# Kernel tuning notes

Hardware: AMD Instinct MI355X
Metric: run time of the kernel (lower is better)

The kernel has to match this reference:

```python
import jax, jax.numpy as jnp
import numpy as np

HEADS = 8
KS = 7
PAD = 3


def grouped_conv1x1(x, w):
    # x: (B, Cin, H, W), w: (heads, Cout/h, Cin/h) -> (B, Cout, H, W)
    B, Cin, H, W = x.shape
    g, co, ci = w.shape
    xg = x.reshape(B, g, ci, H, W)
    out = jnp.einsum('bgchw,goc->bgohw', xg, w)
    return out.reshape(B, g * co, H, W)


def unfold2d(p, k):
    # p: (B, C, Hp, Wp) -> (B, C, H, W, k, k) sliding windows, stride 1
    B, C, Hp, Wp = p.shape
    H, W = Hp - k + 1, Wp - k + 1
    rows = [jnp.stack([p[:, :, i:i + H, j:j + W] for j in range(k)], axis=-1)
            for i in range(k)]
    return jnp.stack(rows, axis=-2)  # (B,C,H,W,k,k)


def setup_inputs() -> dict:
    key = jax.random.key(0)
    ks = jax.random.split(key, 7)
    B, Cin, H, W = 8, 64, 64, 64
    Cout = 64
    g = HEADS
    return {
        'x': jax.random.normal(ks[0], (B, Cin, H, W), jnp.float32),
        'r': jax.random.normal(ks[1], (1,), jnp.float32),
        'w_q': jax.random.normal(ks[2], (g, Cout // g, Cin // g), jnp.float32) * 0.2,
        'w_k': jax.random.normal(ks[3], (g, Cout // g, Cin // g), jnp.float32) * 0.2,
        'w_v': jax.random.normal(ks[4], (g, Cout // g, Cin // g), jnp.float32) * 0.2,
        'rel_h': jax.random.normal(ks[5], (Cout // 2, KS), jnp.float32),
        'rel_w': jax.random.normal(ks[6], (Cout // 2, KS), jnp.float32),
    }


def reference(x, r, w_q, w_k, w_v, rel_h, rel_w):
    B, Cin, H, W = x.shape
    g = HEADS
    Cout = w_q.shape[0] * w_q.shape[1]
    dh = Cout // g

    padded = jnp.pad(x, ((0, 0), (0, 0), (PAD, PAD), (PAD, PAD)))
    q = grouped_conv1x1(x, w_q)            # (B, Cout, H, W)
    k = grouped_conv1x1(padded, w_k)       # (B, Cout, H+2p, W+2p)
    v = grouped_conv1x1(padded, w_v)

    k = unfold2d(k, KS)                    # (B, Cout, H, W, KS, KS)
    v = unfold2d(v, KS)

    # learnable relative positional encoding: split channels in half,
    # add rel_h along window-height, rel_w along window-width
    half = Cout // 2
    k_h = k[:, :half] + rel_h[None, :, None, None, :, None]
    k_w = k[:, half:] + rel_w[None, :, None, None, None, :]
    k = jnp.concatenate([k_h, k_w], axis=1)

    K2 = KS * KS
    k = k.reshape(B, g, dh, H, W, K2)
    v = v.reshape(B, g, dh, H, W, K2)
    q = q.reshape(B, g, dh, H, W, 1)

    scale = np.sqrt(g / Cout).astype(np.float32)
    logits = (q * k).sum(axis=2, keepdims=True) * scale   # (B,g,1,H,W,K2)
    attn = jax.nn.softmax(logits, axis=-1)
    out = (attn * v).sum(axis=-1)                          # (B,g,dh,H,W)
    return out.reshape(B, Cout, H, W)
```

## Files before the change

kernel.cpp:

```cpp
#include <hip/hip_runtime.h>
#include <math.h>

#define NG  8
#define DH  8
#define NCP 4
#define KS  7
#define PAD 3
#define TH  16
#define TW  32
#define OW  2
#define TPH 22
#define RSTW 40
#define PLW  (TPH * RSTW)
#define CH  64
#define HH  64
#define WW  64

typedef __fp16 h2v __attribute__((ext_vector_type(2)));
typedef __fp16 h4v __attribute__((ext_vector_type(4)));

#if __has_builtin(__builtin_amdgcn_exp2f)
#define EXP2(x) __builtin_amdgcn_exp2f(x)
#else
#define EXP2(x) exp2f(x)
#endif

__device__ __forceinline__ int imin(int a, int b) { return a < b ? a : b; }
__device__ __forceinline__ int imax(int a, int b) { return a > b ? a : b; }

__global__ __launch_bounds__(256, 2)
void saconv_kernel(const float* __restrict__ x,
                   const float* __restrict__ wq,
                   const float* __restrict__ wk,
                   const float* __restrict__ wv,
                   const float* __restrict__ relh,
                   const float* __restrict__ relw,
                   float* __restrict__ out) {
  __shared__ h2v xs2[NCP * PLW];
  __shared__ h2v swq2[DH * NCP];
  __shared__ h2v swv2[DH * NCP];
  __shared__ h2v swk2[DH * NCP];
  __shared__ h2v srel2[KS * NCP];

  const int tx  = threadIdx.x;
  const int ty  = threadIdx.y;
  const int tid = ty * 16 + tx;
  const int bz  = blockIdx.z;
  const int b   = bz >> 3;
  const int g   = bz & 7;
  const int h0  = blockIdx.y * TH;
  const int w0  = blockIdx.x * TW;

  const float sl2e = 0.35355339059327373f * 1.4426950408889634f;

  if (tid < 32) {
    int c = tid >> 2, cp = tid & 3;
    swq2[tid] = __builtin_amdgcn_cvt_pkrtz(wq[g * 64 + c * 8 + 2 * cp],
                                           wq[g * 64 + c * 8 + 2 * cp + 1]);
  } else if (tid < 64) {
    int t2 = tid - 32;
    int c = t2 >> 2, cp = t2 & 3;
    swv2[t2] = __builtin_amdgcn_cvt_pkrtz(wv[g * 64 + c * 8 + 2 * cp],
                                          wv[g * 64 + c * 8 + 2 * cp + 1]);
  } else if (tid < 96) {
    int t2 = tid - 64;
    int ci = t2 >> 2, cP = t2 & 3;
    swk2[t2] = __builtin_amdgcn_cvt_pkrtz(wk[g * 64 + (2 * cP) * 8 + ci] * sl2e,
                                          wk[g * 64 + (2 * cP + 1) * 8 + ci] * sl2e);
  } else if (tid < 96 + KS * NCP) {
    int t2 = tid - 96;
    int t = t2 >> 2, cP = t2 & 3;
    float a0, a1;
    if (g < 4) {
      a0 = relh[(g * 8 + 2 * cP) * KS + t];
      a1 = relh[(g * 8 + 2 * cP + 1) * KS + t];
    } else {
      a0 = relw[((g - 4) * 8 + 2 * cP) * KS + t];
      a1 = relw[((g - 4) * 8 + 2 * cP + 1) * KS + t];
    }
    srel2[t2] = __builtin_amdgcn_cvt_pkrtz(a0 * sl2e, a1 * sl2e);
  }

  const float* xb = x + (size_t)(b * CH + g * DH) * (HH * WW);
  const int NCHK = NCP * TPH * 19;
  #pragma unroll
  for (int kk = 0; kk < 7; kk++) {
    int f = tid + kk * 256;
    if (f < NCHK) {
      int cp  = f / (TPH * 19);
      int r   = f - cp * (TPH * 19);
      int row = r / 19;
      int cc  = r - row * 19;
      int yy  = h0 + row - PAD;
      int cy  = imin(imax(yy, 0), HH - 1);
      bool yok = (yy >= 0) & (yy < HH);
      const float* p0 = xb + ((size_t)(2 * cp) * HH + cy) * WW;
      float v0[2], v1[2];
      #pragma unroll
      for (int e = 0; e < 2; e++) {
        int xx = w0 + 2 * cc + e - PAD;
        int cx = imin(imax(xx, 0), WW - 1);
        bool inb = yok & (xx >= 0) & (xx < WW);
        float a0 = p0[cx];
        float a1 = p0[HH * WW + cx];
        v0[e] = inb ? a0 : 0.0f;
        v1[e] = inb ? a1 : 0.0f;
      }
      h2v pk0 = __builtin_amdgcn_cvt_pkrtz(v0[0], v1[0]);
      h2v pk1 = __builtin_amdgcn_cvt_pkrtz(v0[1], v1[1]);
      h4v w4 = { pk0.x, pk0.y, pk1.x, pk1.y };
      *(h4v*)&xs2[cp * PLW + row * RSTW + 2 * cc] = w4;
    }
  }
  __syncthreads();

  __builtin_amdgcn_s_setprio(1);

  h2v  qkh[OW][NCP];
  float rq[OW][KS];
  {
    h2v xc2[OW][NCP];
    #pragma unroll
    for (int o = 0; o < OW; o++)
      #pragma unroll
      for (int cp = 0; cp < NCP; cp++)
        xc2[o][cp] = xs2[cp * PLW + (ty + PAD) * RSTW + (2 * tx + o + PAD)];

    #pragma unroll
    for (int o = 0; o < OW; o++) {
      float q_[DH];
      #pragma unroll
      for (int c = 0; c < DH; c++) {
        float a = 0.f;
        #pragma unroll
        for (int cp = 0; cp < NCP; cp++)
          a = __builtin_amdgcn_fdot2(swq2[c * 4 + cp], xc2[o][cp], a, false);
        q_[c] = a;
      }
      h2v qp[NCP];
      #pragma unroll
      for (int cP = 0; cP < NCP; cP++)
        qp[cP] = __builtin_amdgcn_cvt_pkrtz(q_[2 * cP], q_[2 * cP + 1]);

      float qkt[DH];
      #pragma unroll
      for (int ci = 0; ci < DH; ci++) {
        float a = 0.f;
        #pragma unroll
        for (int cP = 0; cP < NCP; cP++)
          a = __builtin_amdgcn_fdot2(qp[cP], swk2[ci * 4 + cP], a, false);
        qkt[ci] = a;
      }
      #pragma unroll
      for (int cp = 0; cp < NCP; cp++)
        qkh[o][cp] = __builtin_amdgcn_cvt_pkrtz(qkt[2 * cp], qkt[2 * cp + 1]);

      #pragma unroll
      for (int t = 0; t < KS; t++) {
        float a = 0.f;
        #pragma unroll
        for (int cP = 0; cP < NCP; cP++)
          a = __builtin_amdgcn_fdot2(qp[cP], srel2[t * 4 + cP], a, false);
        rq[o][t] = a;
      }
    }
  }

  float s[OW], xa[OW][DH];
  #pragma unroll
  for (int o = 0; o < OW; o++) {
    s[o] = 0.f;
    #pragma unroll
    for (int ci = 0; ci < DH; ci++) xa[o][ci] = 0.f;
  }

#define WINLOOP(DINIT)                                                         \
  _Pragma("unroll")                                                            \
  for (int i = 0; i < KS; i++) {                                               \
    const int wbase = (ty + i) * RSTW + 2 * tx;                                \
    h2v xw[NCP][8];                                                            \
    _Pragma("unroll")                                                          \
    for (int cp = 0; cp < NCP; cp++) {                                         \
      const h4v* bp = (const h4v*)&xs2[cp * PLW + wbase];                      \
      h4v r0 = bp[0], r1 = bp[1], r2 = bp[2], r3 = bp[3];                      \
      xw[cp][0] = __builtin_shufflevector(r0, r0, 0, 1);                       \
      xw[cp][1] = __builtin_shufflevector(r0, r0, 2, 3);                       \
      xw[cp][2] = __builtin_shufflevector(r1, r1, 0, 1);                       \
      xw[cp][3] = __builtin_shufflevector(r1, r1, 2, 3);                       \
      xw[cp][4] = __builtin_shufflevector(r2, r2, 0, 1);                       \
      xw[cp][5] = __builtin_shufflevector(r2, r2, 2, 3);                       \
      xw[cp][6] = __builtin_shufflevector(r3, r3, 0, 1);                       \
      xw[cp][7] = __builtin_shufflevector(r3, r3, 2, 3);                       \
    }                                                                          \
    _Pragma("unroll")                                                          \
    for (int o = 0; o < OW; o++) {                                             \
      float e[KS];                                                             \
      float se = 0.f;                                                          \
      _Pragma("unroll")                                                        \
      for (int j = 0; j < KS; j++) {                                           \
        float d = (DINIT);                                                     \
        _Pragma("unroll")                                                      \
        for (int cp = 0; cp < NCP; cp++)                                       \
          d = __builtin_amdgcn_fdot2(qkh[o][cp], xw[cp][o + j], d, false);     \
        e[j] = EXP2(d);                                                        \
        se += e[j];                                                            \
      }                                                                        \
      s[o] += se;                                                              \
      _Pragma("unroll")                                                        \
      for (int cp = 0; cp < NCP; cp++) {                                       \
        float a0 = xa[o][2 * cp];                                              \
        float a1 = xa[o][2 * cp + 1];                                          \
        _Pragma("unroll")                                                      \
        for (int j = 0; j < KS; j++) {                                         \
          a0 = fmaf(e[j], (float)xw[cp][o + j].x, a0);                         \
          a1 = fmaf(e[j], (float)xw[cp][o + j].y, a1);                         \
        }                                                                      \
        xa[o][2 * cp]     = a0;                                                \
        xa[o][2 * cp + 1] = a1;                                                \
      }                                                                        \
    }                                                                          \
  }

  if (g < 4) { WINLOOP(rq[o][i]) }
  else       { WINLOOP(rq[o][j]) }
#undef WINLOOP

  h2v xav2[OW][NCP];
  #pragma unroll
  for (int o = 0; o < OW; o++) {
    float inv = 1.0f / s[o];
    #pragma unroll
    for (int cp = 0; cp < NCP; cp++)
      xav2[o][cp] = __builtin_amdgcn_cvt_pkrtz(xa[o][2 * cp] * inv,
                                               xa[o][2 * cp + 1] * inv);
  }

  __builtin_amdgcn_s_setprio(0);

  const int h = h0 + ty;
  const int wbase = w0 + 2 * tx;
  #pragma unroll
  for (int c = 0; c < DH; c++) {
    float a0 = 0.f, a1 = 0.f;
    #pragma unroll
    for (int cp = 0; cp < NCP; cp++) {
      a0 = __builtin_amdgcn_fdot2(swv2[c * 4 + cp], xav2[0][cp], a0, false);
      a1 = __builtin_amdgcn_fdot2(swv2[c * 4 + cp], xav2[1][cp], a1, false);
    }
    *(float2*)(&out[((size_t)(b * CH + g * DH + c) * HH + h) * WW + wbase]) =
        make_float2(a0, a1);
  }
}

extern "C" void kernel_launch(void* const* d_in, const int* in_sizes, int n_in,
                              void* d_out, int out_size, void* d_ws, size_t ws_size,
                              hipStream_t stream) {
  const float* x    = (const float*)d_in[0];
  const float* wq   = (const float*)d_in[2];
  const float* wk   = (const float*)d_in[3];
  const float* wv   = (const float*)d_in[4];
  const float* relh = (const float*)d_in[5];
  const float* relw = (const float*)d_in[6];
  float* out = (float*)d_out;

  const int B = in_sizes[0] / (CH * HH * WW);
  dim3 grid(WW / TW, HH / TH, B * NG);
  dim3 block(16, 16, 1);
  saconv_kernel<<<grid, block, 0, stream>>>(x, wq, wk, wv, relh, relw, out);
}
```

Measured before the change: 17.07 us.

## Use packed fp16 dot products for value accumulation via per-channel LDS copy

Adds a second LDS copy of the input tile laid out per channel, with pairs of adjacent columns packed. The attention weights are packed to fp16 pairs, so the value accumulation uses fdot2 over window columns instead of scalar fp32 FMAs with conversions. The logits are also shifted by a constant -8 to keep the exponentials in fp16 range, relying on cancellation in the normalisation. This trades extra LDS space and stores, which may lower occupancy, and reduced precision of the weights for fewer ALU instructions.

```diff
diff --git a/kernel.cpp b/kernel.cpp
--- a/kernel.cpp
+++ b/kernel.cpp
@@ -12,6 +12,8 @@
 #define TPH 22
 #define RSTW 40
 #define PLW  (TPH * RSTW)
+#define RST1 20
+#define PL1  (TPH * RST1)
 #define CH  64
 #define HH  64
 #define WW  64
@@ -37,6 +39,7 @@
                    const float* __restrict__ relw,
                    float* __restrict__ out) {
   __shared__ h2v xs2[NCP * PLW];
+  __shared__ h2v xs1[DH * PL1];
   __shared__ h2v swq2[DH * NCP];
   __shared__ h2v swv2[DH * NCP];
   __shared__ h2v swk2[DH * NCP];
@@ -110,6 +113,8 @@
       h2v pk1 = __builtin_amdgcn_cvt_pkrtz(v0[1], v1[1]);
       h4v w4 = { pk0.x, pk0.y, pk1.x, pk1.y };
       *(h4v*)&xs2[cp * PLW + row * RSTW + 2 * cc] = w4;
+      xs1[(2 * cp) * PL1 + row * RST1 + cc]     = __builtin_amdgcn_cvt_pkrtz(v0[0], v0[1]);
+      xs1[(2 * cp + 1) * PL1 + row * RST1 + cc] = __builtin_amdgcn_cvt_pkrtz(v1[0], v1[1]);
     }
   }
   __syncthreads();
@@ -161,7 +166,7 @@
         #pragma unroll
         for (int cP = 0; cP < NCP; cP++)
           a = __builtin_amdgcn_fdot2(qp[cP], srel2[t * 4 + cP], a, false);
-        rq[o][t] = a;
+        rq[o][t] = a - 8.0f;
       }
     }
   }
@@ -177,7 +182,8 @@
 #define WINLOOP(DINIT)                                                         \
   _Pragma("unroll")                                                            \
   for (int i = 0; i < KS; i++) {                                               \
-    const int wbase = (ty + i) * RSTW + 2 * tx;                                \
+    const int row = ty + i;                                                    \
+    const int wbase = row * RSTW + 2 * tx;                                     \
     h2v xw[NCP][8];                                                            \
     _Pragma("unroll")                                                          \
     for (int cp = 0; cp < NCP; cp++) {                                         \
@@ -192,6 +198,7 @@
       xw[cp][6] = __builtin_shufflevector(r3, r3, 0, 1);                       \
       xw[cp][7] = __builtin_shufflevector(r3, r3, 2, 3);                       \
     }                                                                          \
+    h2v ep[OW][4];                                                             \
     _Pragma("unroll")                                                          \
     for (int o = 0; o < OW; o++) {                                             \
       float e[KS];                                                             \
@@ -206,18 +213,35 @@
         se += e[j];                                                            \
       }                                                                        \
       s[o] += se;                                                              \
-      _Pragma("unroll")                                                        \
-      for (int cp = 0; cp < NCP; cp++) {                                       \
-        float a0 = xa[o][2 * cp];                                              \
-        float a1 = xa[o][2 * cp + 1];                                          \
-        _Pragma("unroll")                                                      \
-        for (int j = 0; j < KS; j++) {                                         \
-          a0 = fmaf(e[j], (float)xw[cp][o + j].x, a0);                         \
-          a1 = fmaf(e[j], (float)xw[cp][o + j].y, a1);                         \
-        }                                                                      \
-        xa[o][2 * cp]     = a0;                                                \
-        xa[o][2 * cp + 1] = a1;                                                \
+      if (o == 0) {                                                            \
+        ep[0][0] = __builtin_amdgcn_cvt_pkrtz(e[0], e[1]);                     \
+        ep[0][1] = __builtin_amdgcn_cvt_pkrtz(e[2], e[3]);                     \
+        ep[0][2] = __builtin_amdgcn_cvt_pkrtz(e[4], e[5]);                     \
+        ep[0][3] = __builtin_amdgcn_cvt_pkrtz(e[6], 0.0f);                     \
+      } else {                                                                 \
+        ep[1][0] = __builtin_amdgcn_cvt_pkrtz(0.0f, e[0]);                     \
+        ep[1][1] = __builtin_amdgcn_cvt_pkrtz(e[1], e[2]);                     \
+        ep[1][2] = __builtin_amdgcn_cvt_pkrtz(e[3], e[4]);                     \
+        ep[1][3] = __builtin_amdgcn_cvt_pkrtz(e[5], e[6]);                     \
       }                                                                        \
+    }                                                                          \
+              \
+    _Pragma("unroll")                                                          \
+    for (int ci = 0; ci < DH; ci++) {                                          \
+      const h2v* jp = &xs1[ci * PL1 + row * RST1 + tx];                        \
+      h2v xj0 = jp[0], xj1 = jp[1], xj2 = jp[2], xj3 = jp[3];                  \
+      float a0 = xa[0][ci];                                                    \
+      a0 = __builtin_amdgcn_fdot2(ep[0][0], xj0, a0, false);                   \
+      a0 = __builtin_amdgcn_fdot2(ep[0][1], xj1, a0, false);                   \
+      a0 = __builtin_amdgcn_fdot2(ep[0][2], xj2, a0, false);                   \
+      a0 = __builtin_amdgcn_fdot2(ep[0][3], xj3, a0, false);                   \
+      xa[0][ci] = a0;                                                          \
+      float a1 = xa[1][ci];                                                    \
+      a1 = __builtin_amdgcn_fdot2(ep[1][0], xj0, a1, false);                   \
+      a1 = __builtin_amdgcn_fdot2(ep[1][1], xj1, a1, false);                   \
+      a1 = __builtin_amdgcn_fdot2(ep[1][2], xj2, a1, false);                   \
+      a1 = __builtin_amdgcn_fdot2(ep[1][3], xj3, a1, false);                   \
+      xa[1][ci] = a1;                                                          \
     }                                                                          \
   }
 
```

After: 18.14 us. 1.06x slower.
